# Kernel optimization log

Measured on AMD Instinct MI355X. Metric: run time of the kernel, lower is better.

Reference implementation:

```python
import jax, jax.numpy as jnp
import numpy as np

N_NODES = 50000
N_EDGES = 800000
IN_DIM = 128
HID_DIM = 128
BN_EPS = 1e-5


def setup_inputs() -> dict:
    key = jax.random.key(0)
    ks = jax.random.split(key, 16)
    s = 0.02
    inp = {
        "h": jax.random.normal(ks[0], (N_NODES, IN_DIM), jnp.float32),
        "x": jax.random.normal(ks[1], (N_NODES, 3), jnp.float32),
        "e": jax.random.randint(ks[2], (2, N_EDGES), 0, N_NODES, jnp.int32),
        # BatchNorm affine params
        "bn_gamma": jnp.ones((IN_DIM,), jnp.float32),
        "bn_beta": jnp.zeros((IN_DIM,), jnp.float32),
        # f_e: Linear(2*in+1 -> hid), SiLU, Linear(hid -> hid), SiLU
        "fe_w1": jax.random.normal(ks[3], (HID_DIM, 2 * IN_DIM + 1), jnp.float32) * s,
        "fe_b1": jnp.zeros((HID_DIM,), jnp.float32),
        "fe_w2": jax.random.normal(ks[4], (HID_DIM, HID_DIM), jnp.float32) * s,
        "fe_b2": jnp.zeros((HID_DIM,), jnp.float32),
        # f_inf: Linear(hid -> 1), Sigmoid
        "finf_w": jax.random.normal(ks[5], (1, HID_DIM), jnp.float32) * s,
        "finf_b": jnp.zeros((1,), jnp.float32),
        # f_h: Linear(in+hid -> hid), SiLU, Linear(hid -> hid)
        "fh_w1": jax.random.normal(ks[6], (HID_DIM, IN_DIM + HID_DIM), jnp.float32) * s,
        "fh_b1": jnp.zeros((HID_DIM,), jnp.float32),
        "fh_w2": jax.random.normal(ks[7], (HID_DIM, HID_DIM), jnp.float32) * s,
        "fh_b2": jnp.zeros((HID_DIM,), jnp.float32),
    }
    return inp


def reference(h, x, e, bn_gamma, bn_beta, fe_w1, fe_b1, fe_w2, fe_b2,
              finf_w, finf_b, fh_w1, fh_b1, fh_w2, fh_b2):
    # BatchNorm1d (training-mode batch stats, biased variance)
    mean = jnp.mean(h, axis=0)
    var = jnp.var(h, axis=0)
    h = (h - mean) * jax.lax.rsqrt(var + BN_EPS) * bn_gamma + bn_beta

    e_st, e_end = e[0], e[1]
    # pairwise distances per edge: [E, 1]
    diff = x[e_st] - x[e_end]
    dists = jnp.sqrt(jnp.sum(diff * diff, axis=1, keepdims=True))

    # edge message MLP f_e on [E, 2*in+1]
    tmp = jnp.concatenate([h[e_st], h[e_end], dists], axis=1)
    m_ij = jax.nn.silu(tmp @ fe_w1.T + fe_b1)
    m_ij = jax.nn.silu(m_ij @ fe_w2.T + fe_b2)

    # gate f_inf: [E, 1]
    e_ij = jax.nn.sigmoid(m_ij @ finf_w.T + finf_b)

    # gated scatter-sum aggregation over source index e[0]
    m_i = jax.ops.segment_sum(e_ij * m_ij, e_st, num_segments=h.shape[0])

    # node update f_h with residual
    u = jax.nn.silu(jnp.concatenate([h, m_i], axis=1) @ fh_w1.T + fh_b1)
    h = h + (u @ fh_w2.T + fh_b2)
    return (h, e)
```

## Files before the change

### kernel.cpp

```cpp
#include <hip/hip_runtime.h>
#include <math.h>

#define N_NODES 50000
#define N_EDGES 800000
#define DIM 128
#define EB 64
#define SCAN_B 196

typedef __attribute__((ext_vector_type(8))) short short8v;
typedef __attribute__((ext_vector_type(4))) float f32x4;

__device__ __forceinline__ float silu_f(float v) { return __fdividef(v, 1.f + __expf(-v)); }

__device__ __forceinline__ unsigned short f2bf(float f) {
  unsigned u = __float_as_uint(f);
  return (unsigned short)((u + 0x7fffu + ((u >> 16) & 1u)) >> 16);
}

__global__ void bn_stats_kernel(const float* __restrict__ h, float* __restrict__ stats) {
  const int c = threadIdx.x & 127;
  const int rs = threadIdx.x >> 7;
  float s = 0.f, s2 = 0.f;
  for (int row = blockIdx.x * 2 + rs; row < N_NODES; row += gridDim.x * 2) {
    float v = h[(size_t)row * DIM + c];
    s += v;
    s2 += v * v;
  }
  __shared__ float red[256];
  red[threadIdx.x] = s;
  __syncthreads();
  if (threadIdx.x < 128) atomicAdd(&stats[c], red[c] + red[c + 128]);
  __syncthreads();
  red[threadIdx.x] = s2;
  __syncthreads();
  if (threadIdx.x < 128) atomicAdd(&stats[DIM + c], red[c] + red[c + 128]);
}

__global__ void bn_finalize_kernel(float* __restrict__ stats, const float* __restrict__ gamma,
                                   const float* __restrict__ beta) {
  const int c = threadIdx.x;
  const float inv_n = 1.f / (float)N_NODES;
  float mean = stats[c] * inv_n;
  float var = stats[DIM + c] * inv_n - mean * mean;
  float s = gamma[c] * rsqrtf(var + 1e-5f);
  stats[2 * DIM + c] = s;
  stats[3 * DIM + c] = beta[c] - mean * s;
}

__global__ void bn_apply_bf_kernel(const float* __restrict__ h, const float* __restrict__ stats,
                                   unsigned short* __restrict__ hbf) {
  const int i4 = blockIdx.x * blockDim.x + threadIdx.x;
  if (i4 >= N_NODES * DIM / 4) return;
  const int c4 = i4 & 31;
  const float4 v = ((const float4*)h)[i4];
  const float4 a = ((const float4*)(stats + 2 * DIM))[c4];
  const float4 b = ((const float4*)(stats + 3 * DIM))[c4];
  ushort4 o;
  o.x = f2bf(v.x * a.x + b.x);
  o.y = f2bf(v.y * a.y + b.y);
  o.z = f2bf(v.z * a.z + b.z);
  o.w = f2bf(v.w * a.w + b.w);
  ((ushort4*)hbf)[i4] = o;
}

__global__ void prep_weights_kernel(const float* __restrict__ fe_w1, const float* __restrict__ fe_w2,
                                    const float* __restrict__ fh_w1, const float* __restrict__ fh_w2,
                                    unsigned short* __restrict__ w1bf, float* __restrict__ w1col,
                                    unsigned short* __restrict__ w2bf, unsigned short* __restrict__ fw1bf,
                                    unsigned short* __restrict__ fw2bf) {
  int idx = blockIdx.x * blockDim.x + threadIdx.x;
  if (idx < 32768) {
    int o = idx >> 8, k = idx & 255;
    w1bf[idx] = f2bf(fe_w1[(size_t)o * 257 + k]);
    return;
  }
  idx -= 32768;
  if (idx < 128) { w1col[idx] = fe_w1[(size_t)idx * 257 + 256]; return; }
  idx -= 128;
  if (idx < 16384) { w2bf[idx] = f2bf(fe_w2[idx]); return; }
  idx -= 16384;
  if (idx < 32768) { fw1bf[idx] = f2bf(fh_w1[idx]); return; }
  idx -= 32768;
  if (idx < 16384) { fw2bf[idx] = f2bf(fh_w2[idx]); return; }
}

__global__ void hist_kernel(const int* __restrict__ e, int* __restrict__ cnt) {
  int i = blockIdx.x * blockDim.x + threadIdx.x;
  if (i < N_EDGES) atomicAdd(&cnt[e[i]], 1);
}

__global__ void scanA_kernel(const int* __restrict__ cnt, int* __restrict__ bsum) {
  __shared__ int red[256];
  const int t = threadIdx.x;
  const int i = blockIdx.x * 256 + t;
  red[t] = (i < N_NODES) ? cnt[i] : 0;
  __syncthreads();
  for (int off = 128; off > 0; off >>= 1) {
    if (t < off) red[t] += red[t + off];
    __syncthreads();
  }
  if (t == 0) bsum[blockIdx.x] = red[0];
}

__global__ void scanB_kernel(int* __restrict__ bsum) {
  __shared__ int s[256];
  const int t = threadIdx.x;
  const int v = (t < SCAN_B) ? bsum[t] : 0;
  s[t] = v;
  __syncthreads();
  for (int off = 1; off < 256; off <<= 1) {
    const int add = (t >= off) ? s[t - off] : 0;
    __syncthreads();
    s[t] += add;
    __syncthreads();
  }
  if (t < SCAN_B) bsum[t] = s[t] - v;
}

__global__ void scanC_kernel(const int* __restrict__ cnt, const int* __restrict__ bsum,
                             int* __restrict__ cursor) {
  __shared__ int s[256];
  const int t = threadIdx.x;
  const int i = blockIdx.x * 256 + t;
  const int v = (i < N_NODES) ? cnt[i] : 0;
  s[t] = v;
  __syncthreads();
  for (int off = 1; off < 256; off <<= 1) {
    const int add = (t >= off) ? s[t - off] : 0;
    __syncthreads();
    s[t] += add;
    __syncthreads();
  }
  if (i < N_NODES) cursor[i] = bsum[blockIdx.x] + s[t] - v;
}

__global__ void sort_scatter_kernel(const int* __restrict__ e, const float* __restrict__ x,
                                    int* __restrict__ cursor, int* __restrict__ srcS,
                                    int* __restrict__ dstS, float* __restrict__ distS) {
  const int i = blockIdx.x * blockDim.x + threadIdx.x;
  if (i >= N_EDGES) return;
  const int s = e[i], d = e[N_EDGES + i];
  const float dx = x[s * 3 + 0] - x[d * 3 + 0];
  const float dy = x[s * 3 + 1] - x[d * 3 + 1];
  const float dz = x[s * 3 + 2] - x[d * 3 + 2];
  const int pos = atomicAdd(&cursor[s], 1);
  srcS[pos] = s;
  dstS[pos] = d;
  distS[pos] = sqrtf(dx * dx + dy * dy + dz * dz);
}

__launch_bounds__(256, 4)
__global__ void edge_mfma_kernel(const unsigned short* __restrict__ hbf,
                                 const int* __restrict__ srcS, const int* __restrict__ dstS,
                                 const float* __restrict__ distS,
                                 const unsigned short* __restrict__ w1bf, const float* __restrict__ w1col,
                                 const float* __restrict__ b1, const unsigned short* __restrict__ w2bf,
                                 const float* __restrict__ b2, const float* __restrict__ winf,
                                 const float* __restrict__ binf, float* __restrict__ mi_g) {
  __shared__ unsigned short Abuf[EB * 256];
  __shared__ int srcs[EB];
  __shared__ int dsts[EB];
  __shared__ float dists[EB];
  __shared__ float gbuf[EB][5];
  __shared__ float gate[EB];

  unsigned short* A2 = Abuf;
  float* Mf = (float*)Abuf;

  const int tid = threadIdx.x;
  const int l = tid & 63, w = tid >> 6;
  const int r16 = l & 15, g = l >> 4;
  const int ebase = blockIdx.x * EB;

  if (tid < EB) {
    srcs[tid] = srcS[ebase + tid];
    dsts[tid] = dstS[ebase + tid];
    dists[tid] = distS[ebase + tid];
  }
  __syncthreads();

  {
    const int er = tid >> 2, cb = (tid & 3) * 8;
    const unsigned short* ps = hbf + (size_t)srcs[er] * DIM;
    const unsigned short* pd = hbf + (size_t)dsts[er] * DIM;
#pragma unroll
    for (int j = 0; j < 8; ++j) {
      const int c = cb + j;
      const int4 v = (c < 16) ? *(const int4*)(ps + c * 8) : *(const int4*)(pd + (c - 16) * 8);
      *(int4*)&Abuf[er * 256 + ((c ^ (er & 7)) << 3)] = v;
    }
  }
  __syncthreads();

  f32x4 acc[4][2];
#pragma unroll
  for (int m_ = 0; m_ < 4; ++m_)
#pragma unroll
    for (int ni = 0; ni < 2; ++ni) acc[m_][ni] = (f32x4){0.f, 0.f, 0.f, 0.f};

  for (int kb = 0; kb < 8; ++kb) {
    short8v a[4], b[2];
#pragma unroll
    for (int m_ = 0; m_ < 4; ++m_) {
      const int er = m_ * 16 + r16;
      const int chunk = kb * 4 + g;
      a[m_] = *(const short8v*)&Abuf[er * 256 + ((chunk ^ (er & 7)) << 3)];
    }
#pragma unroll
    for (int ni = 0; ni < 2; ++ni) {
      const int o = w * 32 + ni * 16 + r16;
      b[ni] = *(const short8v*)&w1bf[o * 256 + kb * 32 + g * 8];
    }
#pragma unroll
    for (int m_ = 0; m_ < 4; ++m_)
#pragma unroll
      for (int ni = 0; ni < 2; ++ni)
        acc[m_][ni] = __builtin_amdgcn_mfma_f32_16x16x32_bf16(a[m_], b[ni], acc[m_][ni], 0, 0, 0);
  }
  __syncthreads();

  {
    const int o0 = w * 32 + r16, o1 = o0 + 16;
    const float wc0 = w1col[o0], wc1 = w1col[o1];
    const float bb0 = b1[o0], bb1 = b1[o1];
#pragma unroll
    for (int m_ = 0; m_ < 4; ++m_)
#pragma unroll
      for (int r = 0; r < 4; ++r) {
        const int er = m_ * 16 + g * 4 + r;
        const float dd = dists[er];
        const float v0 = silu_f(acc[m_][0][r] + dd * wc0 + bb0);
        const float v1 = silu_f(acc[m_][1][r] + dd * wc1 + bb1);
        A2[er * 128 + (o0 ^ ((er & 7) << 3))] = f2bf(v0);
        A2[er * 128 + (o1 ^ ((er & 7) << 3))] = f2bf(v1);
      }
  }
  __syncthreads();

  f32x4 acc2[4][2];
#pragma unroll
  for (int m_ = 0; m_ < 4; ++m_)
#pragma unroll
    for (int ni = 0; ni < 2; ++ni) acc2[m_][ni] = (f32x4){0.f, 0.f, 0.f, 0.f};

  for (int kb = 0; kb < 4; ++kb) {
    short8v a[4], b[2];
    const int k0 = kb * 32 + g * 8;
#pragma unroll
    for (int m_ = 0; m_ < 4; ++m_) {
      const int er = m_ * 16 + r16;
      a[m_] = *(const short8v*)&A2[er * 128 + (k0 ^ ((er & 7) << 3))];
    }
#pragma unroll
    for (int ni = 0; ni < 2; ++ni) {
      const int o = w * 32 + ni * 16 + r16;
      b[ni] = *(const short8v*)&w2bf[o * 128 + k0];
    }
#pragma unroll
    for (int m_ = 0; m_ < 4; ++m_)
#pragma unroll
      for (int ni = 0; ni < 2; ++ni)
        acc2[m_][ni] = __builtin_amdgcn_mfma_f32_16x16x32_bf16(a[m_], b[ni], acc2[m_][ni], 0, 0, 0);
  }

  float m2v[4][2][4];
  float pv[16];
  {
    const int o0 = w * 32 + r16, o1 = o0 + 16;
    const float b20 = b2[o0], b21 = b2[o1];
    const float wf0 = winf[o0], wf1 = winf[o1];
#pragma unroll
    for (int m_ = 0; m_ < 4; ++m_)
#pragma unroll
      for (int r = 0; r < 4; ++r) {
        const float v0 = silu_f(acc2[m_][0][r] + b20);
        const float v1 = silu_f(acc2[m_][1][r] + b21);
        m2v[m_][0][r] = v0;
        m2v[m_][1][r] = v1;
        pv[m_ * 4 + r] = v0 * wf0 + v1 * wf1;
      }
  }

  {
    const bool s0 = r16 & 1;
#pragma unroll
    for (int j = 0; j < 8; ++j) {
      const float lo = pv[2 * j], hi = pv[2 * j + 1];
      const float other = __shfl_xor(s0 ? lo : hi, 1, 64);
      pv[j] = (s0 ? hi : lo) + other;
    }
    const bool s1 = r16 & 2;
#pragma unroll
    for (int j = 0; j < 4; ++j) {
      const float lo = pv[2 * j], hi = pv[2 * j + 1];
      const float other = __shfl_xor(s1 ? lo : hi, 2, 64);
      pv[j] = (s1 ? hi : lo) + other;
    }
    const bool s2 = r16 & 4;
#pragma unroll
    for (int j = 0; j < 2; ++j) {
      const float lo = pv[2 * j], hi = pv[2 * j + 1];
      const float other = __shfl_xor(s2 ? lo : hi, 4, 64);
      pv[j] = (s2 ? hi : lo) + other;
    }
    const bool s3 = r16 & 8;
    {
      const float lo = pv[0], hi = pv[1];
      const float other = __shfl_xor(s3 ? lo : hi, 8, 64);
      pv[0] = (s3 ? hi : lo) + other;
    }
    const int er = (r16 >> 2) * 16 + g * 4 + (r16 & 3);
    gbuf[er][w] = pv[0];
  }
  __syncthreads();
  if (tid < EB) {
    const float s = gbuf[tid][0] + gbuf[tid][1] + gbuf[tid][2] + gbuf[tid][3] + binf[0];
    gate[tid] = __fdividef(1.f, 1.f + __expf(-s));
  }
  __syncthreads();

  {
    const int o0 = w * 32 + r16, o1 = o0 + 16;
#pragma unroll
    for (int m_ = 0; m_ < 4; ++m_)
#pragma unroll
      for (int r = 0; r < 4; ++r) {
        const int er = m_ * 16 + g * 4 + r;
        const float gg = gate[er];
        Mf[er * 128 + (o0 ^ ((er & 7) << 2))] = m2v[m_][0][r] * gg;
        Mf[er * 128 + (o1 ^ ((er & 7) << 2))] = m2v[m_][1][r] * gg;
      }
  }
  __syncthreads();

  {
    const int c = tid & 127;
    const int r0 = (tid >> 7) * 32;
    int cur = srcs[r0];
    float a = 0.f;
    for (int row = r0; row < r0 + 32; ++row) {
      const int s = srcs[row];
      if (s != cur) {
        atomicAdd(&mi_g[(size_t)cur * DIM + c], a);
        a = 0.f;
        cur = s;
      }
      a += Mf[row * 128 + (c ^ ((row & 7) << 2))];
    }
    atomicAdd(&mi_g[(size_t)cur * DIM + c], a);
  }
}

__launch_bounds__(256, 4)
__global__ void node_mfma_kernel(const unsigned short* __restrict__ hbf,
                                 const float* __restrict__ mi_g,
                                 const float* __restrict__ h, const float* __restrict__ stats,
                                 const unsigned short* __restrict__ fw1, const float* __restrict__ fb1,
                                 const unsigned short* __restrict__ fw2, const float* __restrict__ fb2,
                                 float* __restrict__ out) {
  __shared__ unsigned short Abuf[EB * 256];
  unsigned short* A2 = Abuf;

  const int tid = threadIdx.x;
  const int l = tid & 63, w = tid >> 6;
  const int r16 = l & 15, g = l >> 4;
  const int nbase = blockIdx.x * EB;

  {
    const int er = tid >> 2, cb = (tid & 3) * 8;
    int n = nbase + er;
    if (n >= N_NODES) n = N_NODES - 1;
    const unsigned short* ps = hbf + (size_t)n * DIM;
    const float* pm = mi_g + (size_t)n * DIM;
#pragma unroll
    for (int j = 0; j < 8; ++j) {
      const int c = cb + j;
      int4 v;
      if (c < 16) {
        v = *(const int4*)(ps + c * 8);
      } else {
        const float4 f0 = *(const float4*)(pm + (c - 16) * 8);
        const float4 f1 = *(const float4*)(pm + (c - 16) * 8 + 4);
        v.x = (int)f2bf(f0.x) | ((int)f2bf(f0.y) << 16);
        v.y = (int)f2bf(f0.z) | ((int)f2bf(f0.w) << 16);
        v.z = (int)f2bf(f1.x) | ((int)f2bf(f1.y) << 16);
        v.w = (int)f2bf(f1.z) | ((int)f2bf(f1.w) << 16);
      }
      *(int4*)&Abuf[er * 256 + ((c ^ (er & 7)) << 3)] = v;
    }
  }
  __syncthreads();

  f32x4 acc[4][2];
#pragma unroll
  for (int m_ = 0; m_ < 4; ++m_)
#pragma unroll
    for (int ni = 0; ni < 2; ++ni) acc[m_][ni] = (f32x4){0.f, 0.f, 0.f, 0.f};

  for (int kb = 0; kb < 8; ++kb) {
    short8v a[4], b[2];
#pragma unroll
    for (int m_ = 0; m_ < 4; ++m_) {
      const int er = m_ * 16 + r16;
      const int chunk = kb * 4 + g;
      a[m_] = *(const short8v*)&Abuf[er * 256 + ((chunk ^ (er & 7)) << 3)];
    }
#pragma unroll
    for (int ni = 0; ni < 2; ++ni) {
      const int o = w * 32 + ni * 16 + r16;
      b[ni] = *(const short8v*)&fw1[o * 256 + kb * 32 + g * 8];
    }
#pragma unroll
    for (int m_ = 0; m_ < 4; ++m_)
#pragma unroll
      for (int ni = 0; ni < 2; ++ni)
        acc[m_][ni] = __builtin_amdgcn_mfma_f32_16x16x32_bf16(a[m_], b[ni], acc[m_][ni], 0, 0, 0);
  }
  __syncthreads();

  {
    const int o0 = w * 32 + r16, o1 = o0 + 16;
    const float bb0 = fb1[o0], bb1 = fb1[o1];
#pragma unroll
    for (int m_ = 0; m_ < 4; ++m_)
#pragma unroll
      for (int r = 0; r < 4; ++r) {
        const int er = m_ * 16 + g * 4 + r;
        A2[er * 128 + (o0 ^ ((er & 7) << 3))] = f2bf(silu_f(acc[m_][0][r] + bb0));
        A2[er * 128 + (o1 ^ ((er & 7) << 3))] = f2bf(silu_f(acc[m_][1][r] + bb1));
      }
  }
  __syncthreads();

  f32x4 acc2[4][2];
#pragma unroll
  for (int m_ = 0; m_ < 4; ++m_)
#pragma unroll
    for (int ni = 0; ni < 2; ++ni) acc2[m_][ni] = (f32x4){0.f, 0.f, 0.f, 0.f};

  for (int kb = 0; kb < 4; ++kb) {
    short8v a[4], b[2];
    const int k0 = kb * 32 + g * 8;
#pragma unroll
    for (int m_ = 0; m_ < 4; ++m_) {
      const int er = m_ * 16 + r16;
      a[m_] = *(const short8v*)&A2[er * 128 + (k0 ^ ((er & 7) << 3))];
    }
#pragma unroll
    for (int ni = 0; ni < 2; ++ni) {
      const int o = w * 32 + ni * 16 + r16;
      b[ni] = *(const short8v*)&fw2[o * 128 + k0];
    }
#pragma unroll
    for (int m_ = 0; m_ < 4; ++m_)
#pragma unroll
      for (int ni = 0; ni < 2; ++ni)
        acc2[m_][ni] = __builtin_amdgcn_mfma_f32_16x16x32_bf16(a[m_], b[ni], acc2[m_][ni], 0, 0, 0);
  }

#pragma unroll
  for (int ni = 0; ni < 2; ++ni) {
    const int o = w * 32 + ni * 16 + r16;
    const float bb = fb2[o];
    const float sc = stats[2 * DIM + o];
    const float sh = stats[3 * DIM + o];
#pragma unroll
    for (int m_ = 0; m_ < 4; ++m_)
#pragma unroll
      for (int r = 0; r < 4; ++r) {
        const int n = nbase + m_ * 16 + g * 4 + r;
        if (n < N_NODES) {
          const float hv = h[(size_t)n * DIM + o];
          out[(size_t)n * DIM + o] = hv * sc + sh + acc2[m_][ni][r] + bb;
        }
      }
  }
}

__global__ void ecopy_kernel(const int* __restrict__ e, float* __restrict__ out_e) {
  const int i4 = blockIdx.x * blockDim.x + threadIdx.x;
  if (i4 >= 2 * N_EDGES / 4) return;
  const int4 v = ((const int4*)e)[i4];
  float4 o;
  o.x = (float)v.x;
  o.y = (float)v.y;
  o.z = (float)v.z;
  o.w = (float)v.w;
  ((float4*)out_e)[i4] = o;
}

extern "C" void kernel_launch(void* const* d_in, const int* in_sizes, int n_in, void* d_out,
                              int out_size, void* d_ws, size_t ws_size, hipStream_t stream) {
  const float* h = (const float*)d_in[0];
  const float* x = (const float*)d_in[1];
  const int* e = (const int*)d_in[2];
  const float* bn_gamma = (const float*)d_in[3];
  const float* bn_beta = (const float*)d_in[4];
  const float* fe_w1 = (const float*)d_in[5];
  const float* fe_b1 = (const float*)d_in[6];
  const float* fe_w2 = (const float*)d_in[7];
  const float* fe_b2 = (const float*)d_in[8];
  const float* finf_w = (const float*)d_in[9];
  const float* finf_b = (const float*)d_in[10];
  const float* fh_w1 = (const float*)d_in[11];
  const float* fh_b1 = (const float*)d_in[12];
  const float* fh_w2 = (const float*)d_in[13];
  const float* fh_b2 = (const float*)d_in[14];

  char* wp = (char*)d_ws;
  auto alloc = [&](size_t bytes) -> char* {
    char* p = wp;
    wp += (bytes + 255) & ~(size_t)255;
    return p;
  };
  float* stats = (float*)alloc(512 * sizeof(float));
  unsigned short* hbf = (unsigned short*)alloc((size_t)N_NODES * DIM * 2);
  unsigned short* w1bf = (unsigned short*)alloc(128 * 256 * 2);
  float* w1col = (float*)alloc(128 * 4);
  unsigned short* w2bf = (unsigned short*)alloc(128 * 128 * 2);
  unsigned short* fw1bf = (unsigned short*)alloc(128 * 256 * 2);
  unsigned short* fw2bf = (unsigned short*)alloc(128 * 128 * 2);
  int* cnt = (int*)alloc((size_t)N_NODES * 4);
  int* cursor = (int*)alloc((size_t)N_NODES * 4);
  int* bsum = (int*)alloc((size_t)SCAN_B * 4);
  int* srcS = (int*)alloc((size_t)N_EDGES * 4);
  int* dstS = (int*)alloc((size_t)N_EDGES * 4);
  float* distS = (float*)alloc((size_t)N_EDGES * 4);
  float* mi_g = (float*)alloc((size_t)N_NODES * DIM * 4);

  float* out = (float*)d_out;
  float* out_e = out + (size_t)N_NODES * DIM;

  hipMemsetAsync(stats, 0, 512 * sizeof(float), stream);
  hipMemsetAsync(cnt, 0, N_NODES * sizeof(int), stream);
  hipMemsetAsync(mi_g, 0, (size_t)N_NODES * DIM * sizeof(float), stream);

  bn_stats_kernel<<<256, 256, 0, stream>>>(h, stats);
  bn_finalize_kernel<<<1, 128, 0, stream>>>(stats, bn_gamma, bn_beta);
  bn_apply_bf_kernel<<<(N_NODES * DIM / 4 + 255) / 256, 256, 0, stream>>>(h, stats, hbf);
  prep_weights_kernel<<<(98432 + 255) / 256, 256, 0, stream>>>(fe_w1, fe_w2, fh_w1, fh_w2, w1bf,
                                                               w1col, w2bf, fw1bf, fw2bf);
  hist_kernel<<<(N_EDGES + 255) / 256, 256, 0, stream>>>(e, cnt);
  scanA_kernel<<<SCAN_B, 256, 0, stream>>>(cnt, bsum);
  scanB_kernel<<<1, 256, 0, stream>>>(bsum);
  scanC_kernel<<<SCAN_B, 256, 0, stream>>>(cnt, bsum, cursor);
  sort_scatter_kernel<<<(N_EDGES + 255) / 256, 256, 0, stream>>>(e, x, cursor, srcS, dstS, distS);

  edge_mfma_kernel<<<N_EDGES / EB, 256, 0, stream>>>(hbf, srcS, dstS, distS, w1bf, w1col, fe_b1,
                                                     w2bf, fe_b2, finf_w, finf_b, mi_g);
  node_mfma_kernel<<<(N_NODES + EB - 1) / EB, 256, 0, stream>>>(hbf, mi_g, h, stats, fw1bf, fh_b1,
                                                                fw2bf, fh_b2, out);
  ecopy_kernel<<<(2 * N_EDGES / 4 + 255) / 256, 256, 0, stream>>>(e, out_e);
}
```

Baseline: 492.6 us.

## Merge prep kernels by block range and halve MFMA-kernel LDS for occupancy

Small preparation kernels (BN stats, histogram, edge copy, weight conversion; finalize with scanA; scanC with BN apply and mi_g zeroing) are combined into block-range-dispatched launches, and two memsets become one. This removes several launch boundaries and lets independent work overlap. The edge and node MFMA kernels now stage src/dst (or h/m_i) halves one after another in a 64x128 LDS buffer, allowing launch bounds of 6 blocks per SM instead of 4. The gated message buffer is now stored as bf16 before the segment reduction, which adds rounding error in exchange for smaller shared memory.

```diff
diff --git a/kernel.cpp b/kernel.cpp
--- a/kernel.cpp
+++ b/kernel.cpp
@@ -6,6 +6,12 @@
 #define DIM 128
 #define EB 64
 #define SCAN_B 196
+#define BN_B 256
+#define HIST_B 3125
+#define ECOPY_B 1563
+#define PREP_B 385
+#define APPLY_B 6250
+#define MIZ_B 6250
 
 typedef __attribute__((ext_vector_type(8))) short short8v;
 typedef __attribute__((ext_vector_type(4))) float f32x4;
@@ -17,58 +23,54 @@
   return (unsigned short)((u + 0x7fffu + ((u >> 16) & 1u)) >> 16);
 }
 
-__global__ void bn_stats_kernel(const float* __restrict__ h, float* __restrict__ stats) {
-  const int c = threadIdx.x & 127;
-  const int rs = threadIdx.x >> 7;
-  float s = 0.f, s2 = 0.f;
-  for (int row = blockIdx.x * 2 + rs; row < N_NODES; row += gridDim.x * 2) {
-    float v = h[(size_t)row * DIM + c];
-    s += v;
-    s2 += v * v;
-  }
+__global__ void k1_fused_kernel(const float* __restrict__ h, const int* __restrict__ e,
+                                const float* __restrict__ fe_w1, const float* __restrict__ fe_w2,
+                                const float* __restrict__ fh_w1, const float* __restrict__ fh_w2,
+                                float* __restrict__ stats, int* __restrict__ cnt,
+                                float* __restrict__ out_e, unsigned short* __restrict__ w1bf,
+                                float* __restrict__ w1col, unsigned short* __restrict__ w2bf,
+                                unsigned short* __restrict__ fw1bf, unsigned short* __restrict__ fw2bf) {
   __shared__ float red[256];
-  red[threadIdx.x] = s;
-  __syncthreads();
-  if (threadIdx.x < 128) atomicAdd(&stats[c], red[c] + red[c + 128]);
-  __syncthreads();
-  red[threadIdx.x] = s2;
-  __syncthreads();
-  if (threadIdx.x < 128) atomicAdd(&stats[DIM + c], red[c] + red[c + 128]);
-}
-
-__global__ void bn_finalize_kernel(float* __restrict__ stats, const float* __restrict__ gamma,
-                                   const float* __restrict__ beta) {
-  const int c = threadIdx.x;
-  const float inv_n = 1.f / (float)N_NODES;
-  float mean = stats[c] * inv_n;
-  float var = stats[DIM + c] * inv_n - mean * mean;
-  float s = gamma[c] * rsqrtf(var + 1e-5f);
-  stats[2 * DIM + c] = s;
-  stats[3 * DIM + c] = beta[c] - mean * s;
-}
-
-__global__ void bn_apply_bf_kernel(const float* __restrict__ h, const float* __restrict__ stats,
-                                   unsigned short* __restrict__ hbf) {
-  const int i4 = blockIdx.x * blockDim.x + threadIdx.x;
-  if (i4 >= N_NODES * DIM / 4) return;
-  const int c4 = i4 & 31;
-  const float4 v = ((const float4*)h)[i4];
-  const float4 a = ((const float4*)(stats + 2 * DIM))[c4];
-  const float4 b = ((const float4*)(stats + 3 * DIM))[c4];
-  ushort4 o;
-  o.x = f2bf(v.x * a.x + b.x);
-  o.y = f2bf(v.y * a.y + b.y);
-  o.z = f2bf(v.z * a.z + b.z);
-  o.w = f2bf(v.w * a.w + b.w);
-  ((ushort4*)hbf)[i4] = o;
-}
-
-__global__ void prep_weights_kernel(const float* __restrict__ fe_w1, const float* __restrict__ fe_w2,
-                                    const float* __restrict__ fh_w1, const float* __restrict__ fh_w2,
-                                    unsigned short* __restrict__ w1bf, float* __restrict__ w1col,
-                                    unsigned short* __restrict__ w2bf, unsigned short* __restrict__ fw1bf,
-                                    unsigned short* __restrict__ fw2bf) {
-  int idx = blockIdx.x * blockDim.x + threadIdx.x;
+  const int bid = blockIdx.x;
+  const int tid = threadIdx.x;
+
+  if (bid < BN_B) {
+    const int c = tid & 127;
+    const int rs = tid >> 7;
+    float s = 0.f, s2 = 0.f;
+    for (int row = bid * 2 + rs; row < N_NODES; row += BN_B * 2) {
+      float v = h[(size_t)row * DIM + c];
+      s += v;
+      s2 += v * v;
+    }
+    red[tid] = s;
+    __syncthreads();
+    if (tid < 128) atomicAdd(&stats[c], red[c] + red[c + 128]);
+    __syncthreads();
+    red[tid] = s2;
+    __syncthreads();
+    if (tid < 128) atomicAdd(&stats[DIM + c], red[c] + red[c + 128]);
+    return;
+  }
+  if (bid < BN_B + HIST_B) {
+    const int i = (bid - BN_B) * 256 + tid;
+    if (i < N_EDGES) atomicAdd(&cnt[e[i]], 1);
+    return;
+  }
+  if (bid < BN_B + HIST_B + ECOPY_B) {
+    const int i4 = (bid - BN_B - HIST_B) * 256 + tid;
+    if (i4 < 2 * N_EDGES / 4) {
+      const int4 v = ((const int4*)e)[i4];
+      float4 o;
+      o.x = (float)v.x;
+      o.y = (float)v.y;
+      o.z = (float)v.z;
+      o.w = (float)v.w;
+      ((float4*)out_e)[i4] = o;
+    }
+    return;
+  }
+  int idx = (bid - BN_B - HIST_B - ECOPY_B) * 256 + tid;
   if (idx < 32768) {
     int o = idx >> 8, k = idx & 255;
     w1bf[idx] = f2bf(fe_w1[(size_t)o * 257 + k]);
@@ -84,22 +86,31 @@
   if (idx < 16384) { fw2bf[idx] = f2bf(fh_w2[idx]); return; }
 }
 
-__global__ void hist_kernel(const int* __restrict__ e, int* __restrict__ cnt) {
-  int i = blockIdx.x * blockDim.x + threadIdx.x;
-  if (i < N_EDGES) atomicAdd(&cnt[e[i]], 1);
-}
-
-__global__ void scanA_kernel(const int* __restrict__ cnt, int* __restrict__ bsum) {
+__global__ void k2_fused_kernel(const int* __restrict__ cnt, int* __restrict__ bsum,
+                                float* __restrict__ stats, const float* __restrict__ gamma,
+                                const float* __restrict__ beta) {
   __shared__ int red[256];
+  const int bid = blockIdx.x;
   const int t = threadIdx.x;
-  const int i = blockIdx.x * 256 + t;
-  red[t] = (i < N_NODES) ? cnt[i] : 0;
-  __syncthreads();
-  for (int off = 128; off > 0; off >>= 1) {
-    if (t < off) red[t] += red[t + off];
+  if (bid < SCAN_B) {
+    const int i = bid * 256 + t;
+    red[t] = (i < N_NODES) ? cnt[i] : 0;
     __syncthreads();
-  }
-  if (t == 0) bsum[blockIdx.x] = red[0];
+    for (int off = 128; off > 0; off >>= 1) {
+      if (t < off) red[t] += red[t + off];
+      __syncthreads();
+    }
+    if (t == 0) bsum[bid] = red[0];
+    return;
+  }
+  if (t < 128) {
+    const float inv_n = 1.f / (float)N_NODES;
+    float mean = stats[t] * inv_n;
+    float var = stats[DIM + t] * inv_n - mean * mean;
+    float s = gamma[t] * rsqrtf(var + 1e-5f);
+    stats[2 * DIM + t] = s;
+    stats[3 * DIM + t] = beta[t] - mean * s;
+  }
 }
 
 __global__ void scanB_kernel(int* __restrict__ bsum) {
@@ -117,21 +128,43 @@
   if (t < SCAN_B) bsum[t] = s[t] - v;
 }
 
-__global__ void scanC_kernel(const int* __restrict__ cnt, const int* __restrict__ bsum,
-                             int* __restrict__ cursor) {
+__global__ void k3_fused_kernel(const int* __restrict__ cnt, const int* __restrict__ bsum,
+                                int* __restrict__ cursor, const float* __restrict__ h,
+                                const float* __restrict__ stats, unsigned short* __restrict__ hbf,
+                                float* __restrict__ mi_g) {
   __shared__ int s[256];
+  const int bid = blockIdx.x;
   const int t = threadIdx.x;
-  const int i = blockIdx.x * 256 + t;
-  const int v = (i < N_NODES) ? cnt[i] : 0;
-  s[t] = v;
-  __syncthreads();
-  for (int off = 1; off < 256; off <<= 1) {
-    const int add = (t >= off) ? s[t - off] : 0;
+  if (bid < SCAN_B) {
+    const int i = bid * 256 + t;
+    const int v = (i < N_NODES) ? cnt[i] : 0;
+    s[t] = v;
     __syncthreads();
-    s[t] += add;
-    __syncthreads();
-  }
-  if (i < N_NODES) cursor[i] = bsum[blockIdx.x] + s[t] - v;
+    for (int off = 1; off < 256; off <<= 1) {
+      const int add = (t >= off) ? s[t - off] : 0;
+      __syncthreads();
+      s[t] += add;
+      __syncthreads();
+    }
+    if (i < N_NODES) cursor[i] = bsum[bid] + s[t] - v;
+    return;
+  }
+  if (bid < SCAN_B + APPLY_B) {
+    const int i4 = (bid - SCAN_B) * 256 + t;
+    const int c4 = i4 & 31;
+    const float4 v = ((const float4*)h)[i4];
+    const float4 a = ((const float4*)(stats + 2 * DIM))[c4];
+    const float4 b = ((const float4*)(stats + 3 * DIM))[c4];
+    ushort4 o;
+    o.x = f2bf(v.x * a.x + b.x);
+    o.y = f2bf(v.y * a.y + b.y);
+    o.z = f2bf(v.z * a.z + b.z);
+    o.w = f2bf(v.w * a.w + b.w);
+    ((ushort4*)hbf)[i4] = o;
+    return;
+  }
+  const int i4 = (bid - SCAN_B - APPLY_B) * 256 + t;
+  ((float4*)mi_g)[i4] = (float4){0.f, 0.f, 0.f, 0.f};
 }
 
 __global__ void sort_scatter_kernel(const int* __restrict__ e, const float* __restrict__ x,
@@ -149,7 +182,7 @@
   distS[pos] = sqrtf(dx * dx + dy * dy + dz * dz);
 }
 
-__launch_bounds__(256, 4)
+__launch_bounds__(256, 6)
 __global__ void edge_mfma_kernel(const unsigned short* __restrict__ hbf,
                                  const int* __restrict__ srcS, const int* __restrict__ dstS,
                                  const float* __restrict__ distS,
@@ -157,16 +190,13 @@
                                  const float* __restrict__ b1, const unsigned short* __restrict__ w2bf,
                                  const float* __restrict__ b2, const float* __restrict__ winf,
                                  const float* __restrict__ binf, float* __restrict__ mi_g) {
-  __shared__ unsigned short Abuf[EB * 256];
+  __shared__ unsigned short buf[EB * 128];
   __shared__ int srcs[EB];
   __shared__ int dsts[EB];
   __shared__ float dists[EB];
   __shared__ float gbuf[EB][5];
   __shared__ float gate[EB];
 
-  unsigned short* A2 = Abuf;
-  float* Mf = (float*)Abuf;
-
   const int tid = threadIdx.x;
   const int l = tid & 63, w = tid >> 6;
   const int r16 = l & 15, g = l >> 4;
@@ -179,15 +209,14 @@
   }
   __syncthreads();
 
-  {
-    const int er = tid >> 2, cb = (tid & 3) * 8;
-    const unsigned short* ps = hbf + (size_t)srcs[er] * DIM;
-    const unsigned short* pd = hbf + (size_t)dsts[er] * DIM;
-#pragma unroll
-    for (int j = 0; j < 8; ++j) {
-      const int c = cb + j;
-      const int4 v = (c < 16) ? *(const int4*)(ps + c * 8) : *(const int4*)(pd + (c - 16) * 8);
-      *(int4*)&Abuf[er * 256 + ((c ^ (er & 7)) << 3)] = v;
+  const int er_s = tid >> 2, cb_s = (tid & 3) * 4;
+
+  {
+    const unsigned short* ps = hbf + (size_t)srcs[er_s] * DIM;
+#pragma unroll
+    for (int j = 0; j < 4; ++j) {
+      const int c = cb_s + j;
+      *(int4*)&buf[er_s * 128 + ((c ^ (er_s & 7)) << 3)] = *(const int4*)(ps + c * 8);
     }
   }
   __syncthreads();
@@ -198,13 +227,13 @@
 #pragma unroll
     for (int ni = 0; ni < 2; ++ni) acc[m_][ni] = (f32x4){0.f, 0.f, 0.f, 0.f};
 
-  for (int kb = 0; kb < 8; ++kb) {
+#pragma unroll
+  for (int kb = 0; kb < 4; ++kb) {
     short8v a[4], b[2];
 #pragma unroll
     for (int m_ = 0; m_ < 4; ++m_) {
       const int er = m_ * 16 + r16;
-      const int chunk = kb * 4 + g;
-      a[m_] = *(const short8v*)&Abuf[er * 256 + ((chunk ^ (er & 7)) << 3)];
+      a[m_] = *(const short8v*)&buf[er * 128 + (((kb * 4 + g) ^ (er & 7)) << 3)];
     }
 #pragma unroll
     for (int ni = 0; ni < 2; ++ni) {
@@ -220,6 +249,37 @@
   __syncthreads();
 
   {
+    const unsigned short* pd = hbf + (size_t)dsts[er_s] * DIM;
+#pragma unroll
+    for (int j = 0; j < 4; ++j) {
+      const int c = cb_s + j;
+      *(int4*)&buf[er_s * 128 + ((c ^ (er_s & 7)) << 3)] = *(const int4*)(pd + c * 8);
+    }
+  }
+  __syncthreads();
+
+#pragma unroll
+  for (int kb = 4; kb < 8; ++kb) {
+    short8v a[4], b[2];
+#pragma unroll
+    for (int m_ = 0; m_ < 4; ++m_) {
+      const int er = m_ * 16 + r16;
+      a[m_] = *(const short8v*)&buf[er * 128 + ((((kb - 4) * 4 + g) ^ (er & 7)) << 3)];
+    }
+#pragma unroll
+    for (int ni = 0; ni < 2; ++ni) {
+      const int o = w * 32 + ni * 16 + r16;
+      b[ni] = *(const short8v*)&w1bf[o * 256 + kb * 32 + g * 8];
+    }
+#pragma unroll
+    for (int m_ = 0; m_ < 4; ++m_)
+#pragma unroll
+      for (int ni = 0; ni < 2; ++ni)
+        acc[m_][ni] = __builtin_amdgcn_mfma_f32_16x16x32_bf16(a[m_], b[ni], acc[m_][ni], 0, 0, 0);
+  }
+  __syncthreads();
+
+  {
     const int o0 = w * 32 + r16, o1 = o0 + 16;
     const float wc0 = w1col[o0], wc1 = w1col[o1];
     const float bb0 = b1[o0], bb1 = b1[o1];
@@ -229,10 +289,8 @@
       for (int r = 0; r < 4; ++r) {
         const int er = m_ * 16 + g * 4 + r;
         const float dd = dists[er];
-        const float v0 = silu_f(acc[m_][0][r] + dd * wc0 + bb0);
-        const float v1 = silu_f(acc[m_][1][r] + dd * wc1 + bb1);
-        A2[er * 128 + (o0 ^ ((er & 7) << 3))] = f2bf(v0);
-        A2[er * 128 + (o1 ^ ((er & 7) << 3))] = f2bf(v1);
+        buf[er * 128 + (o0 ^ ((er & 7) << 3))] = f2bf(silu_f(acc[m_][0][r] + dd * wc0 + bb0));
+        buf[er * 128 + (o1 ^ ((er & 7) << 3))] = f2bf(silu_f(acc[m_][1][r] + dd * wc1 + bb1));
       }
   }
   __syncthreads();
@@ -243,13 +301,14 @@
 #pragma unroll
     for (int ni = 0; ni < 2; ++ni) acc2[m_][ni] = (f32x4){0.f, 0.f, 0.f, 0.f};
 
+#pragma unroll
   for (int kb = 0; kb < 4; ++kb) {
     short8v a[4], b[2];
     const int k0 = kb * 32 + g * 8;
 #pragma unroll
     for (int m_ = 0; m_ < 4; ++m_) {
       const int er = m_ * 16 + r16;
-      a[m_] = *(const short8v*)&A2[er * 128 + (k0 ^ ((er & 7) << 3))];
+      a[m_] = *(const short8v*)&buf[er * 128 + (k0 ^ ((er & 7) << 3))];
     }
 #pragma unroll
     for (int ni = 0; ni < 2; ++ni) {
@@ -263,7 +322,6 @@
         acc2[m_][ni] = __builtin_amdgcn_mfma_f32_16x16x32_bf16(a[m_], b[ni], acc2[m_][ni], 0, 0, 0);
   }
 
-  float m2v[4][2][4];
   float pv[16];
   {
     const int o0 = w * 32 + r16, o1 = o0 + 16;
@@ -275,8 +333,8 @@
       for (int r = 0; r < 4; ++r) {
         const float v0 = silu_f(acc2[m_][0][r] + b20);
         const float v1 = silu_f(acc2[m_][1][r] + b21);
-        m2v[m_][0][r] = v0;
-        m2v[m_][1][r] = v1;
+        acc2[m_][0][r] = v0;
+        acc2[m_][1][r] = v1;
         pv[m_ * 4 + r] = v0 * wf0 + v1 * wf1;
       }
   }
@@ -327,8 +385,8 @@
       for (int r = 0; r < 4; ++r) {
         const int er = m_ * 16 + g * 4 + r;
         const float gg = gate[er];
-        Mf[er * 128 + (o0 ^ ((er & 7) << 2))] = m2v[m_][0][r] * gg;
-        Mf[er * 128 + (o1 ^ ((er & 7) << 2))] = m2v[m_][1][r] * gg;
+        buf[er * 128 + (o0 ^ ((er & 7) << 3))] = f2bf(acc2[m_][0][r] * gg);
+        buf[er * 128 + (o1 ^ ((er & 7) << 3))] = f2bf(acc2[m_][1][r] * gg);
       }
   }
   __syncthreads();
@@ -345,48 +403,36 @@
         a = 0.f;
         cur = s;
       }
-      a += Mf[row * 128 + (c ^ ((row & 7) << 2))];
+      a += __uint_as_float((unsigned)buf[row * 128 + (c ^ ((row & 7) << 3))] << 16);
     }
     atomicAdd(&mi_g[(size_t)cur * DIM + c], a);
   }
 }
 
-__launch_bounds__(256, 4)
+__launch_bounds__(256, 6)
 __global__ void node_mfma_kernel(const unsigned short* __restrict__ hbf,
                                  const float* __restrict__ mi_g,
                                  const float* __restrict__ h, const float* __restrict__ stats,
                                  const unsigned short* __restrict__ fw1, const float* __restrict__ fb1,
                                  const unsigned short* __restrict__ fw2, const float* __restrict__ fb2,
                                  float* __restrict__ out) {
-  __shared__ unsigned short Abuf[EB * 256];
-  unsigned short* A2 = Abuf;
+  __shared__ unsigned short buf[EB * 128];
 
   const int tid = threadIdx.x;
   const int l = tid & 63, w = tid >> 6;
   const int r16 = l & 15, g = l >> 4;
   const int nbase = blockIdx.x * EB;
 
-  {
-    const int er = tid >> 2, cb = (tid & 3) * 8;
-    int n = nbase + er;
-    if (n >= N_NODES) n = N_NODES - 1;
-    const unsigned short* ps = hbf + (size_t)n * DIM;
-    const float* pm = mi_g + (size_t)n * DIM;
-#pragma unroll
-    for (int j = 0; j < 8; ++j) {
-      const int c = cb + j;
-      int4 v;
-      if (c < 16) {
-        v = *(const int4*)(ps + c * 8);
-      } else {
-        const float4 f0 = *(const float4*)(pm + (c - 16) * 8);
-        const float4 f1 = *(const float4*)(pm + (c - 16) * 8 + 4);
-        v.x = (int)f2bf(f0.x) | ((int)f2bf(f0.y) << 16);
-        v.y = (int)f2bf(f0.z) | ((int)f2bf(f0.w) << 16);
-        v.z = (int)f2bf(f1.x) | ((int)f2bf(f1.y) << 16);
-        v.w = (int)f2bf(f1.z) | ((int)f2bf(f1.w) << 16);
-      }
-      *(int4*)&Abuf[er * 256 + ((c ^ (er & 7)) << 3)] = v;
+  const int er_s = tid >> 2, cb_s = (tid & 3) * 4;
+  int nstg = nbase + er_s;
+  if (nstg >= N_NODES) nstg = N_NODES - 1;
+
+  {
+    const unsigned short* ps = hbf + (size_t)nstg * DIM;
+#pragma unroll
+    for (int j = 0; j < 4; ++j) {
+      const int c = cb_s + j;
+      *(int4*)&buf[er_s * 128 + ((c ^ (er_s & 7)) << 3)] = *(const int4*)(ps + c * 8);
     }
   }
   __syncthreads();
@@ -397,13 +443,13 @@
 #pragma unroll
     for (int ni = 0; ni < 2; ++ni) acc[m_][ni] = (f32x4){0.f, 0.f, 0.f, 0.f};
 
-  for (int kb = 0; kb < 8; ++kb) {
+#pragma unroll
+  for (int kb = 0; kb < 4; ++kb) {
     short8v a[4], b[2];
 #pragma unroll
     for (int m_ = 0; m_ < 4; ++m_) {
       const int er = m_ * 16 + r16;
-      const int chunk = kb * 4 + g;
-      a[m_] = *(const short8v*)&Abuf[er * 256 + ((chunk ^ (er & 7)) << 3)];
+      a[m_] = *(const short8v*)&buf[er * 128 + (((kb * 4 + g) ^ (er & 7)) << 3)];
     }
 #pragma unroll
     for (int ni = 0; ni < 2; ++ni) {
@@ -419,6 +465,44 @@
   __syncthreads();
 
   {
+    const float* pm = mi_g + (size_t)nstg * DIM;
+#pragma unroll
+    for (int j = 0; j < 4; ++j) {
+      const int c = cb_s + j;
+      const float4 f0 = *(const float4*)(pm + c * 8);
+      const float4 f1 = *(const float4*)(pm + c * 8 + 4);
+      int4 v;
+      v.x = (int)f2bf(f0.x) | ((int)f2bf(f0.y) << 16);
+      v.y = (int)f2bf(f0.z) | ((int)f2bf(f0.w) << 16);
+      v.z = (int)f2bf(f1.x) | ((int)f2bf(f1.y) << 16);
+      v.w = (int)f2bf(f1.z) | ((int)f2bf(f1.w) << 16);
+      *(int4*)&buf[er_s * 128 + ((c ^ (er_s & 7)) << 3)] = v;
+    }
+  }
+  __syncthreads();
+
+#pragma unroll
+  for (int kb = 4; kb < 8; ++kb) {
+    short8v a[4], b[2];
+#pragma unroll
+    for (int m_ = 0; m_ < 4; ++m_) {
+      const int er = m_ * 16 + r16;
+      a[m_] = *(const short8v*)&buf[er * 128 + ((((kb - 4) * 4 + g) ^ (er & 7)) << 3)];
+    }
+#pragma unroll
+    for (int ni = 0; ni < 2; ++ni) {
+      const int o = w * 32 + ni * 16 + r16;
+      b[ni] = *(const short8v*)&fw1[o * 256 + kb * 32 + g * 8];
+    }
+#pragma unroll
+    for (int m_ = 0; m_ < 4; ++m_)
+#pragma unroll
+      for (int ni = 0; ni < 2; ++ni)
+        acc[m_][ni] = __builtin_amdgcn_mfma_f32_16x16x32_bf16(a[m_], b[ni], acc[m_][ni], 0, 0, 0);
+  }
+  __syncthreads();
+
+  {
     const int o0 = w * 32 + r16, o1 = o0 + 16;
     const float bb0 = fb1[o0], bb1 = fb1[o1];
 #pragma unroll
@@ -426,8 +510,8 @@
 #pragma unroll
       for (int r = 0; r < 4; ++r) {
         const int er = m_ * 16 + g * 4 + r;
-        A2[er * 128 + (o0 ^ ((er & 7) << 3))] = f2bf(silu_f(acc[m_][0][r] + bb0));
-        A2[er * 128 + (o1 ^ ((er & 7) << 3))] = f2bf(silu_f(acc[m_][1][r] + bb1));
+        buf[er * 128 + (o0 ^ ((er & 7) << 3))] = f2bf(silu_f(acc[m_][0][r] + bb0));
+        buf[er * 128 + (o1 ^ ((er & 7) << 3))] = f2bf(silu_f(acc[m_][1][r] + bb1));
       }
   }
   __syncthreads();
@@ -438,13 +522,14 @@
 #pragma unroll
     for (int ni = 0; ni < 2; ++ni) acc2[m_][ni] = (f32x4){0.f, 0.f, 0.f, 0.f};
 
+#pragma unroll
   for (int kb = 0; kb < 4; ++kb) {
     short8v a[4], b[2];
     const int k0 = kb * 32 + g * 8;
 #pragma unroll
     for (int m_ = 0; m_ < 4; ++m_) {
       const int er = m_ * 16 + r16;
-      a[m_] = *(const short8v*)&A2[er * 128 + (k0 ^ ((er & 7) << 3))];
+      a[m_] = *(const short8v*)&buf[er * 128 + (k0 ^ ((er & 7) << 3))];
     }
 #pragma unroll
     for (int ni = 0; ni < 2; ++ni) {
@@ -475,18 +560,6 @@
         }
       }
   }
-}
-
-__global__ void ecopy_kernel(const int* __restrict__ e, float* __restrict__ out_e) {
-  const int i4 = blockIdx.x * blockDim.x + threadIdx.x;
-  if (i4 >= 2 * N_EDGES / 4) return;
-  const int4 v = ((const int4*)e)[i4];
-  float4 o;
-  o.x = (float)v.x;
-  o.y = (float)v.y;
-  o.z = (float)v.z;
-  o.w = (float)v.w;
-  ((float4*)out_e)[i4] = o;
 }
 
 extern "C" void kernel_launch(void* const* d_in, const int* in_sizes, int n_in, void* d_out,
@@ -514,13 +587,13 @@
     return p;
   };
   float* stats = (float*)alloc(512 * sizeof(float));
+  int* cnt = (int*)alloc((size_t)N_NODES * 4);
   unsigned short* hbf = (unsigned short*)alloc((size_t)N_NODES * DIM * 2);
   unsigned short* w1bf = (unsigned short*)alloc(128 * 256 * 2);
   float* w1col = (float*)alloc(128 * 4);
   unsigned short* w2bf = (unsigned short*)alloc(128 * 128 * 2);
   unsigned short* fw1bf = (unsigned short*)alloc(128 * 256 * 2);
   unsigned short* fw2bf = (unsigned short*)alloc(128 * 128 * 2);
-  int* cnt = (int*)alloc((size_t)N_NODES * 4);
   int* cursor = (int*)alloc((size_t)N_NODES * 4);
   int* bsum = (int*)alloc((size_t)SCAN_B * 4);
   int* srcS = (int*)alloc((size_t)N_EDGES * 4);
@@ -531,24 +604,17 @@
   float* out = (float*)d_out;
   float* out_e = out + (size_t)N_NODES * DIM;
 
-  hipMemsetAsync(stats, 0, 512 * sizeof(float), stream);
-  hipMemsetAsync(cnt, 0, N_NODES * sizeof(int), stream);
-  hipMemsetAsync(mi_g, 0, (size_t)N_NODES * DIM * sizeof(float), stream);
-
-  bn_stats_kernel<<<256, 256, 0, stream>>>(h, stats);
-  bn_finalize_kernel<<<1, 128, 0, stream>>>(stats, bn_gamma, bn_beta);
-  bn_apply_bf_kernel<<<(N_NODES * DIM / 4 + 255) / 256, 256, 0, stream>>>(h, stats, hbf);
-  prep_weights_kernel<<<(98432 + 255) / 256, 256, 0, stream>>>(fe_w1, fe_w2, fh_w1, fh_w2, w1bf,
-                                                               w1col, w2bf, fw1bf, fw2bf);
-  hist_kernel<<<(N_EDGES + 255) / 256, 256, 0, stream>>>(e, cnt);
-  scanA_kernel<<<SCAN_B, 256, 0, stream>>>(cnt, bsum);
+  hipMemsetAsync(stats, 0, 2048 + (size_t)N_NODES * 4, stream);
+
+  k1_fused_kernel<<<BN_B + HIST_B + ECOPY_B + PREP_B, 256, 0, stream>>>(
+      h, e, fe_w1, fe_w2, fh_w1, fh_w2, stats, cnt, out_e, w1bf, w1col, w2bf, fw1bf, fw2bf);
+  k2_fused_kernel<<<SCAN_B + 1, 256, 0, stream>>>(cnt, bsum, stats, bn_gamma, bn_beta);
   scanB_kernel<<<1, 256, 0, stream>>>(bsum);
-  scanC_kernel<<<SCAN_B, 256, 0, stream>>>(cnt, bsum, cursor);
+  k3_fused_kernel<<<SCAN_B + APPLY_B + MIZ_B, 256, 0, stream>>>(cnt, bsum, cursor, h, stats, hbf,
+                                                                mi_g);
   sort_scatter_kernel<<<(N_EDGES + 255) / 256, 256, 0, stream>>>(e, x, cursor, srcS, dstS, distS);
-
   edge_mfma_kernel<<<N_EDGES / EB, 256, 0, stream>>>(hbf, srcS, dstS, distS, w1bf, w1col, fe_b1,
                                                      w2bf, fe_b2, finf_w, finf_b, mi_g);
   node_mfma_kernel<<<(N_NODES + EB - 1) / EB, 256, 0, stream>>>(hbf, mi_g, h, stats, fw1bf, fh_b1,
                                                                 fw2bf, fh_b2, out);
-  ecopy_kernel<<<(2 * N_EDGES / 4 + 255) / 256, 256, 0, stream>>>(e, out_e);
-}
+}
```

Measured after the change: 532.2 us. +8.0%, slower.
